# Kernel optimization log

Measured on AMD Instinct MI355X. Metric: run time of the kernel, lower is better.

The kernel has to match this reference:

```python
import jax, jax.numpy as jnp
import numpy as np

B, N, DIM = 4, 1024, 512
H, DH = 8, 64
INNER = H * DH
MLP = 2048
EPS = 1e-5


def layernorm(x, g, b):
    m = x.mean(-1, keepdims=True)
    v = ((x - m) ** 2).mean(-1, keepdims=True)
    return (x - m) / jnp.sqrt(v + EPS) * g + b


def setup_inputs() -> dict:
    key = jax.random.key(0)
    ks = jax.random.split(key, 12)
    s = 0.02
    return {
        "q": jax.random.normal(ks[0], (B, N, DIM), jnp.float32),
        "k": jax.random.normal(ks[1], (B, N, DIM), jnp.float32),
        "v": jax.random.normal(ks[2], (B, N, DIM), jnp.float32),
        "Win": jax.random.normal(ks[3], (INNER, DIM), jnp.float32) * s,
        "Wout": jax.random.normal(ks[4], (DIM, INNER), jnp.float32) * s,
        "bout": jnp.zeros((DIM,), jnp.float32),
        "g1": jnp.ones((DIM,), jnp.float32),
        "b1n": jnp.zeros((DIM,), jnp.float32),
        "g2": jnp.ones((DIM,), jnp.float32),
        "b2n": jnp.zeros((DIM,), jnp.float32),
        "Wup": jax.random.normal(ks[5], (MLP, DIM), jnp.float32) * s,
        "bup": jnp.zeros((MLP,), jnp.float32),
        "Wdn": jax.random.normal(ks[6], (DIM, MLP), jnp.float32) * s,
        "bdn": jnp.zeros((DIM,), jnp.float32),
        "wp_W1": jax.random.normal(ks[7], (DH, 2 * DH), jnp.float32) * s,
        "wp_b1": jnp.zeros((DH,), jnp.float32),
        "wp_g": jnp.ones((DH,), jnp.float32),
        "wp_b": jnp.zeros((DH,), jnp.float32),
        "wp_W2": jax.random.normal(ks[8], (3, DH), jnp.float32) * s,
        "wp_b2": jnp.zeros((3,), jnp.float32),
        "num_heads": H,
        "dim_head": DH,
        "mlp_dim": MLP,
    }


def reference(q, k, v, Win, Wout, bout, g1, b1n, g2, b2n, Wup, bup, Wdn, bdn,
              wp_W1, wp_b1, wp_g, wp_b, wp_W2, wp_b2, num_heads, dim_head, mlp_dim):
    b, n, _ = q.shape

    def split_heads(x):  # [b,n,dim] -> [h,b,n,d]
        f = x @ Win.T
        return f.reshape(b, n, num_heads, dim_head).transpose(2, 0, 1, 3)

    fq = split_heads(layernorm(q, g1, b1n))
    fk = split_heads(layernorm(k, g1, b1n))
    fv = split_heads(layernorm(v, g1, b1n))

    # cosine similarity component
    dots = jnp.einsum('hbnd,hbmd->hbnm', fq, fk)
    nq = jnp.linalg.norm(fq, axis=-1)  # [h,b,n]
    nk = jnp.linalg.norm(fk, axis=-1)  # [h,b,m]
    cosine_sim = dots / (nq[..., :, None] * nk[..., None, :])

    # mean-centered covariance component
    qc = fq - fq.mean(-1, keepdims=True)
    kc = fk - fk.mean(-1, keepdims=True)
    cov_component = jnp.einsum('hbnd,hbmd->hbnm', qc, kc) / dim_head

    # variance outer-product component (torch.var -> unbiased, ddof=1)
    qv = jnp.var(fq, axis=-1, ddof=1)  # [h,b,n]
    kv = jnp.var(fk, axis=-1, ddof=1)  # [h,b,m]
    var_component = qv[..., :, None] * kv[..., None, :] / dim_head

    # dynamic per-head mixing weights
    qg = fq.mean(axis=(1, 2))  # [h,d]
    kg = fk.mean(axis=(1, 2))
    feats = jnp.concatenate([qg, kg], axis=-1)  # [h,2d]
    h1 = jax.nn.relu(layernorm(feats @ wp_W1.T + wp_b1, wp_g, wp_b))
    w = jax.nn.softmax(h1 @ wp_W2.T + wp_b2, axis=-1)  # [h,3]
    cw = w[:, 0][:, None, None, None]
    covw = w[:, 1][:, None, None, None]
    vw = w[:, 2][:, None, None, None]

    scores = cw * cosine_sim + covw * cov_component + vw * var_component
    out = jnp.einsum('hbnm,hbmd->hbnd', scores, fv)
    out = out.transpose(1, 2, 0, 3).reshape(b, n, num_heads * dim_head)
    attn = out @ Wout.T + bout

    q2 = q + attn
    x = layernorm(q2, g2, b2n)
    y = jax.nn.gelu(x @ Wup.T + bup, approximate=False) @ Wdn.T + bdn
    return q2 + y
```

## Files before the change

### kernel.cpp

```cpp
#include <hip/hip_runtime.h>
#include <math.h>

#define EPS 1e-5f
#define ROWS 4096

typedef __attribute__((ext_vector_type(8))) short short8;
typedef __attribute__((ext_vector_type(4))) float floatx4;

__device__ inline short f2bf(float f) {
    unsigned u = __builtin_bit_cast(unsigned, f);
    unsigned r = (u + 0x7fffu + ((u >> 16) & 1u)) >> 16;
    return (short)r;
}
__device__ inline float bf2f(short s) {
    return __builtin_bit_cast(float, (unsigned)(unsigned short)s << 16);
}

__global__ __launch_bounds__(256) void prep(
    const float* __restrict__ q, const float* __restrict__ k,
    const float* __restrict__ v, const float* __restrict__ g,
    const float* __restrict__ bb, short* __restrict__ qkvout,
    const float* __restrict__ w0, const float* __restrict__ w1,
    const float* __restrict__ w2, const float* __restrict__ w3,
    short* __restrict__ o0, short* __restrict__ o1,
    short* __restrict__ o2, short* __restrict__ o3,
    const float* __restrict__ g2, const float* __restrict__ b2n,
    float* __restrict__ Bn, float* __restrict__ Wg,
    float* __restrict__ zero0) {
    int bx = blockIdx.x;
    int t = threadIdx.x;
    if (bx < 3072) {
        int tensor = bx >> 10;
        int xb = bx & 1023;
        const float* x = tensor == 0 ? q : (tensor == 1 ? k : v);
        int row = xb * 4 + (t >> 6);
        int col = (t & 63) * 8;
        const float* xr = x + (size_t)row * 512 + col;
        float4 v0 = *(const float4*)xr;
        float4 v1 = *(const float4*)(xr + 4);
        float s = v0.x + v0.y + v0.z + v0.w + v1.x + v1.y + v1.z + v1.w;
        float sq = v0.x * v0.x + v0.y * v0.y + v0.z * v0.z + v0.w * v0.w +
                   v1.x * v1.x + v1.y * v1.y + v1.z * v1.z + v1.w * v1.w;
#pragma unroll
        for (int off = 32; off; off >>= 1) {
            s += __shfl_xor(s, off);
            sq += __shfl_xor(sq, off);
        }
        float m = s * (1.f / 512.f);
        float rstd = rsqrtf(sq * (1.f / 512.f) - m * m + EPS);
        float4 g0 = *(const float4*)(g + col);
        float4 g1 = *(const float4*)(g + col + 4);
        float4 b0 = *(const float4*)(bb + col);
        float4 b1 = *(const float4*)(bb + col + 4);
        short8 o;
        o[0] = f2bf((v0.x - m) * rstd * g0.x + b0.x);
        o[1] = f2bf((v0.y - m) * rstd * g0.y + b0.y);
        o[2] = f2bf((v0.z - m) * rstd * g0.z + b0.z);
        o[3] = f2bf((v0.w - m) * rstd * g0.w + b0.w);
        o[4] = f2bf((v1.x - m) * rstd * g1.x + b1.x);
        o[5] = f2bf((v1.y - m) * rstd * g1.y + b1.y);
        o[6] = f2bf((v1.z - m) * rstd * g1.z + b1.z);
        o[7] = f2bf((v1.w - m) * rstd * g1.w + b1.w);
        *(short8*)(qkvout + (size_t)(tensor * 4096 + row) * 512 + col) = o;
        return;
    }
    if (bx < 4352) {
        int wb = bx - 3072;
        if (wb >= 256 && wb < 768) {
            int base = wb - 256;
            int idx = base * 2048 + t * 8;
            int n = idx >> 9, c = idx & 511;
            float4 v0 = *(const float4*)(w2 + idx);
            float4 v1 = *(const float4*)(w2 + idx + 4);
            float4 ga = *(const float4*)(g2 + c);
            float4 gb = *(const float4*)(g2 + c + 4);
            float4 ba = *(const float4*)(b2n + c);
            float4 bbv = *(const float4*)(b2n + c + 4);
            short8 o;
            o[0] = f2bf(ga.x * v0.x); o[1] = f2bf(ga.y * v0.y);
            o[2] = f2bf(ga.z * v0.z); o[3] = f2bf(ga.w * v0.w);
            o[4] = f2bf(gb.x * v1.x); o[5] = f2bf(gb.y * v1.y);
            o[6] = f2bf(gb.z * v1.z); o[7] = f2bf(gb.w * v1.w);
            *(short8*)(o2 + idx) = o;
            float bn = ba.x * v0.x + ba.y * v0.y + ba.z * v0.z + ba.w * v0.w +
                       bbv.x * v1.x + bbv.y * v1.y + bbv.z * v1.z + bbv.w * v1.w;
            float wg = ga.x * v0.x + ga.y * v0.y + ga.z * v0.z + ga.w * v0.w +
                       gb.x * v1.x + gb.y * v1.y + gb.z * v1.z + gb.w * v1.w;
#pragma unroll
            for (int off = 32; off; off >>= 1) {
                bn += __shfl_xor(bn, off);
                wg += __shfl_xor(wg, off);
            }
            if ((t & 63) == 0) {
                Bn[n] = bn;
                Wg[n] = wg;
            }
            return;
        }
        const float* src;
        short* dst;
        int base;
        if (wb < 128) { src = w0; dst = o0; base = wb; }
        else if (wb < 256) { src = w1; dst = o1; base = wb - 128; }
        else { src = w3; dst = o3; base = wb - 768; }
        int idx = base * 2048 + t * 8;
        float4 v0 = *(const float4*)(src + idx);
        float4 v1 = *(const float4*)(src + idx + 4);
        short8 o;
        o[0] = f2bf(v0.x); o[1] = f2bf(v0.y); o[2] = f2bf(v0.z); o[3] = f2bf(v0.w);
        o[4] = f2bf(v1.x); o[5] = f2bf(v1.y); o[6] = f2bf(v1.z); o[7] = f2bf(v1.w);
        *(short8*)(dst + idx) = o;
        return;
    }
    int zi = (bx - 4352) * 1024 + t * 4;
    if (zi < 275456) *(float4*)(zero0 + zi) = (float4){0.f, 0.f, 0.f, 0.f};
}

template <int TM, int TN, int EPI, bool OUT_BF16>
__global__ __launch_bounds__(256) void mfma_gemm_nt(
    const short* __restrict__ A, const short* __restrict__ B,
    void* __restrict__ C, int M, int N, int K,
    const float* __restrict__ bias, const float* __restrict__ resid,
    short* __restrict__ C2, float* __restrict__ Sb,
    float* __restrict__ qgp, float* __restrict__ kgp) {
    constexpr int FI = TM / 32;
    constexpr int FJ = TN / 32;
    __shared__ short As[2][TM * 32];
    __shared__ short Bs[2][TN * 32];
    int t = threadIdx.x;
    int m0 = blockIdx.y * TM, n0 = blockIdx.x * TN;
    int w = t >> 6, lane = t & 63;
    int wm = (w & 1) * (TM / 2), wn = (w >> 1) * (TN / 2);
    floatx4 acc[FI][FJ];
#pragma unroll
    for (int i = 0; i < FI; ++i)
#pragma unroll
        for (int j = 0; j < FJ; ++j) acc[i][j] = (floatx4){0.f, 0.f, 0.f, 0.f};

    int arow = t >> 2, acol = (t & 3) * 8;
    const short* Ag = A + (size_t)(m0 + arow) * K + acol;
    const short* Bg = B + (size_t)(n0 + arow) * K + acol;
    int ldsbase = w * 1024;

    auto stage = [&](int k0, int buf) {
#pragma unroll
        for (int u = 0; u < TM / 64; ++u)
            __builtin_amdgcn_global_load_lds(
                (const __attribute__((address_space(1))) void*)(Ag + (size_t)u * 64 * K + k0),
                (__attribute__((address_space(3))) void*)((char*)As[buf] + u * 4096 + ldsbase),
                16, 0, 0);
#pragma unroll
        for (int u = 0; u < TN / 64; ++u)
            __builtin_amdgcn_global_load_lds(
                (const __attribute__((address_space(1))) void*)(Bg + (size_t)u * 64 * K + k0),
                (__attribute__((address_space(3))) void*)((char*)Bs[buf] + u * 4096 + ldsbase),
                16, 0, 0);
    };

    stage(0, 0);
    __syncthreads();
    int nsteps = K >> 5;
    for (int ks = 0; ks < nsteps; ++ks) {
        int buf = ks & 1;
        if (ks + 1 < nsteps) stage((ks + 1) << 5, buf ^ 1);
        int krow = (lane >> 4) * 8;
        short8 af[FI], bf[FJ];
#pragma unroll
        for (int i = 0; i < FI; ++i)
            af[i] = *(const short8*)&As[buf][(wm + i * 16 + (lane & 15)) * 32 + krow];
#pragma unroll
        for (int j = 0; j < FJ; ++j)
            bf[j] = *(const short8*)&Bs[buf][(wn + j * 16 + (lane & 15)) * 32 + krow];
#pragma unroll
        for (int i = 0; i < FI; ++i)
#pragma unroll
            for (int j = 0; j < FJ; ++j)
                acc[i][j] = __builtin_amdgcn_mfma_f32_16x16x32_bf16(
                    af[i], bf[j], acc[i][j], 0, 0, 0);
        __syncthreads();
    }

    int col = lane & 15, rbase = (lane >> 4) * 4;
    if constexpr (EPI == 5) {
#pragma unroll
        for (int i = 0; i < FI; ++i) {
#pragma unroll
            for (int r = 0; r < 4; ++r) {
                int grow = m0 + wm + i * 16 + rbase + r;
                float s = 0.f, sq = 0.f;
#pragma unroll
                for (int j = 0; j < FJ; ++j) {
                    int gcol = n0 + wn + j * 16 + col;
                    float vv = acc[i][j][r] + bias[gcol] +
                               resid[(size_t)grow * N + gcol];
                    ((float*)C)[(size_t)grow * N + gcol] = vv;
                    C2[(size_t)grow * N + gcol] = f2bf(vv);
                    s += vv;
                    sq += vv * vv;
                }
#pragma unroll
                for (int off = 1; off < 16; off <<= 1) {
                    s += __shfl_xor(s, off);
                    sq += __shfl_xor(sq, off);
                }
                if ((lane & 15) == 0) {
                    atomicAdd(&Sb[grow], s);
                    atomicAdd(&Sb[4096 + grow], sq);
                }
            }
        }
    } else if constexpr (EPI == 4) {
#pragma unroll
        for (int i = 0; i < FI; ++i) {
#pragma unroll
            for (int r = 0; r < 4; ++r) {
                int grow = m0 + wm + i * 16 + rbase + r;
                float m = Sb[grow] * (1.f / 512.f);
                float rstd = rsqrtf(Sb[4096 + grow] * (1.f / 512.f) - m * m + EPS);
                float mrstd = m * rstd;
#pragma unroll
                for (int j = 0; j < FJ; ++j) {
                    int gcol = n0 + wn + j * 16 + col;
                    float vv = rstd * acc[i][j][r] + qgp[gcol] + bias[gcol] -
                               mrstd * kgp[gcol];
                    vv = 0.5f * vv * (1.f + erff(vv * 0.70710678118654752f));
                    ((short*)C)[(size_t)grow * N + gcol] = f2bf(vv);
                }
            }
        }
    } else {
#pragma unroll
        for (int i = 0; i < FI; ++i) {
#pragma unroll
            for (int j = 0; j < FJ; ++j) {
                int gcol = n0 + wn + j * 16 + col;
#pragma unroll
                for (int r = 0; r < 4; ++r) {
                    int grow = m0 + wm + i * 16 + rbase + r;
                    float v = acc[i][j][r];
                    if (EPI == 2) v += bias[gcol] + resid[(size_t)grow * N + gcol];
                    if (OUT_BF16)
                        ((short*)C)[(size_t)grow * N + gcol] = f2bf(v);
                    else
                        ((float*)C)[(size_t)grow * N + gcol] = v;
                }
            }
        }
    }

    if constexpr (EPI == 1) {
        if (m0 < 8192) {
            int tensor = m0 >> 12;
            float* Sbase = Sb + (size_t)tensor * 98304;
            float* dst = tensor ? kgp : qgp;
            int head = (n0 + wn) >> 6;
            int rowbase = (m0 & 4095) + wm;
#pragma unroll
            for (int i = 0; i < FI; ++i) {
#pragma unroll
                for (int r = 0; r < 4; ++r) {
                    float s = 0.f, sq = 0.f;
#pragma unroll
                    for (int j = 0; j < FJ; ++j) {
                        float vv = acc[i][j][r];
                        s += vv;
                        sq += vv * vv;
                    }
#pragma unroll
                    for (int off = 1; off < 16; off <<= 1) {
                        s += __shfl_xor(s, off);
                        sq += __shfl_xor(sq, off);
                    }
                    if ((lane & 15) == 0) {
                        int row = rowbase + i * 16 + rbase + r;
                        int idx = head * ROWS + row;
                        float m = s * (1.f / 64.f);
                        Sbase[idx] = m;
                        Sbase[32768 + idx] = rsqrtf(sq);
                        Sbase[65536 + idx] = (sq - 64.f * m * m) * (1.f / 63.f);
                    }
                }
            }
            float cs[FJ];
#pragma unroll
            for (int j = 0; j < FJ; ++j) {
                float s = 0.f;
#pragma unroll
                for (int i = 0; i < FI; ++i)
#pragma unroll
                    for (int r = 0; r < 4; ++r) s += acc[i][j][r];
                s += __shfl_xor(s, 16);
                s += __shfl_xor(s, 32);
                cs[j] = s;
            }
            if (lane < 16) {
#pragma unroll
                for (int j = 0; j < FJ; ++j)
                    atomicAdd(&dst[head * 64 + j * 16 + lane], cs[j] * (1.f / 4096.f));
            }
        }
    }
}

__global__ __launch_bounds__(256) void tr_kv(
    const short* __restrict__ fkb, const short* __restrict__ fvb,
    const float* __restrict__ rnk, const float* __restrict__ kvv,
    const float* __restrict__ mkm, short* __restrict__ fkTall,
    short* __restrict__ fvT, float* __restrict__ Sv,
    const float* __restrict__ qg, const float* __restrict__ kg,
    const float* __restrict__ W1, const float* __restrict__ b1,
    const float* __restrict__ g, const float* __restrict__ bb,
    const float* __restrict__ W2, const float* __restrict__ b2,
    float* __restrict__ wmix) {
    int hb = blockIdx.x;
    int t = threadIdx.x;
    if (blockIdx.y == 8) {
        if (blockIdx.z != 0 || hb >= 8 || t >= 64) return;
        int h = hb, j = t;
        float acc = 0.f;
        const float* w1r = W1 + j * 128;
        for (int i = 0; i < 64; ++i) acc += qg[h * 64 + i] * w1r[i];
        for (int i = 0; i < 64; ++i) acc += kg[h * 64 + i] * w1r[64 + i];
        acc += b1[j];
        float s = acc, sq = acc * acc;
#pragma unroll
        for (int off = 32; off; off >>= 1) {
            s += __shfl_xor(s, off);
            sq += __shfl_xor(sq, off);
        }
        float m = s * (1.f / 64.f);
        float var = sq * (1.f / 64.f) - m * m;
        float xh = (acc - m) * rsqrtf(var + EPS) * g[j] + bb[j];
        float r = fmaxf(xh, 0.f);
        float l[3];
#pragma unroll
        for (int c = 0; c < 3; ++c) {
            float p = r * W2[c * 64 + j];
#pragma unroll
            for (int off = 32; off; off >>= 1) p += __shfl_xor(p, off);
            l[c] = p + b2[c];
        }
        if (j == 0) {
            float mx = fmaxf(l[0], fmaxf(l[1], l[2]));
            float e0 = expf(l[0] - mx), e1 = expf(l[1] - mx), e2 = expf(l[2] - mx);
            float inv = 1.f / (e0 + e1 + e2);
            wmix[h * 3 + 0] = e0 * inv;
            wmix[h * 3 + 1] = e1 * inv;
            wmix[h * 3 + 2] = e2 * inv;
        }
        return;
    }
    int chunk = blockIdx.y;
    int tensor = blockIdx.z;
    int h = hb >> 2, b = hb & 3;
    __shared__ float tile[32][68];
    __shared__ float sc[32], sc2[32];
    const short* src = tensor ? fvb : fkb;
    float skv_acc = 0.f, smk_acc = 0.f;
    int e = t & 63, qd = t >> 6;
    int d = t >> 2, mg = (t & 3) * 8;
    for (int s4 = 0; s4 < 4; ++s4) {
        int m0 = chunk * 128 + s4 * 32;
        __syncthreads();
        {
            int idx = t * 8;
            int mm = idx >> 6, dd = idx & 63;
            short8 sv = *(const short8*)&src[(size_t)(b * 1024 + m0 + mm) * 512 + h * 64 + dd];
#pragma unroll
            for (int i = 0; i < 8; ++i) tile[mm][dd + i] = bf2f(sv[i]);
        }
        if (t < 32) {
            int sidx = h * ROWS + b * 1024 + m0 + t;
            if (tensor == 0) {
                sc[t] = rnk[sidx];
            } else {
                sc[t] = kvv[sidx];
                sc2[t] = mkm[sidx];
            }
        }
        __syncthreads();
        if (tensor == 0) {
            short8 o1, o2;
#pragma unroll
            for (int i = 0; i < 8; ++i) {
                float vv = tile[mg + i][d];
                o1[i] = f2bf(vv);
                o2[i] = f2bf(vv * sc[mg + i]);
            }
            *(short8*)&fkTall[((size_t)hb * 128 + d) * 1024 + m0 + mg] = o1;
            *(short8*)&fkTall[((size_t)hb * 128 + 64 + d) * 1024 + m0 + mg] = o2;
        } else {
            short8 o1;
#pragma unroll
            for (int i = 0; i < 8; ++i) o1[i] = f2bf(tile[mg + i][d]);
            *(short8*)&fvT[((size_t)hb * 64 + d) * 1024 + m0 + mg] = o1;
#pragma unroll
            for (int i = 0; i < 8; ++i) {
                float vv = tile[qd * 8 + i][e];
                skv_acc += sc[qd * 8 + i] * vv;
                smk_acc += sc2[qd * 8 + i] * vv;
            }
        }
    }
    if (tensor == 1) {
        atomicAdd(&Sv[hb * 128 + e], skv_acc);
        atomicAdd(&Sv[hb * 128 + 64 + e], smk_acc);
    }
}

__global__ __launch_bounds__(256) void kside_gemm(
    const short* __restrict__ fkTall, const short* __restrict__ fvT,
    float* __restrict__ Mnew) {
    int hb = blockIdx.x, half = blockIdx.y, kz = blockIdx.z;
    const short* A = fkTall + ((size_t)hb * 128 + half * 64) * 1024 + kz * 256;
    const short* B = fvT + (size_t)hb * 64 * 1024 + kz * 256;
    __shared__ short As[2][64 * 32];
    __shared__ short Bs[2][64 * 32];
    int t = threadIdx.x;
    int w = t >> 6, lane = t & 63;
    int wm = (w & 1) * 32, wn = (w >> 1) * 32;
    floatx4 acc[2][2];
#pragma unroll
    for (int i = 0; i < 2; ++i)
#pragma unroll
        for (int j = 0; j < 2; ++j) acc[i][j] = (floatx4){0.f, 0.f, 0.f, 0.f};
    int arow = t >> 2, acol = (t & 3) * 8;
    const short* Ag = A + (size_t)arow * 1024 + acol;
    const short* Bg = B + (size_t)arow * 1024 + acol;
    int ldsbase = w * 1024;

    auto stage = [&](int k0, int buf) {
        __builtin_amdgcn_global_load_lds(
            (const __attribute__((address_space(1))) void*)(Ag + k0),
            (__attribute__((address_space(3))) void*)((char*)As[buf] + ldsbase), 16, 0, 0);
        __builtin_amdgcn_global_load_lds(
            (const __attribute__((address_space(1))) void*)(Bg + k0),
            (__attribute__((address_space(3))) void*)((char*)Bs[buf] + ldsbase), 16, 0, 0);
    };

    stage(0, 0);
    __syncthreads();
    for (int ks = 0; ks < 8; ++ks) {
        int buf = ks & 1;
        if (ks + 1 < 8) stage((ks + 1) << 5, buf ^ 1);
        int krow = (lane >> 4) * 8;
        short8 af[2], bf[2];
#pragma unroll
        for (int i = 0; i < 2; ++i)
            af[i] = *(const short8*)&As[buf][(wm + i * 16 + (lane & 15)) * 32 + krow];
#pragma unroll
        for (int j = 0; j < 2; ++j)
            bf[j] = *(const short8*)&Bs[buf][(wn + j * 16 + (lane & 15)) * 32 + krow];
#pragma unroll
        for (int i = 0; i < 2; ++i)
#pragma unroll
            for (int j = 0; j < 2; ++j)
                acc[i][j] = __builtin_amdgcn_mfma_f32_16x16x32_bf16(
                    af[i], bf[j], acc[i][j], 0, 0, 0);
        __syncthreads();
    }
    int col = lane & 15, rbase = (lane >> 4) * 4;
    float* Cb = Mnew + (size_t)hb * 8192 + half * 4096;
#pragma unroll
    for (int i = 0; i < 2; ++i)
#pragma unroll
        for (int j = 0; j < 2; ++j)
#pragma unroll
            for (int r = 0; r < 4; ++r)
                atomicAdd(&Cb[(wm + i * 16 + rbase + r) * 64 + wn + j * 16 + col],
                          acc[i][j][r]);
}

__global__ __launch_bounds__(256) void qside(
    const short* __restrict__ fqb, const float* __restrict__ Mnew,
    const float* __restrict__ Sv, const float* __restrict__ rnq,
    const float* __restrict__ mq, const float* __restrict__ qv,
    const float* __restrict__ wmix, short* __restrict__ attn_out) {
    int ntile = blockIdx.x, hb = blockIdx.y;
    int h = hb >> 2, b = hb & 3;
    __shared__ float M1s[4096], M2s[4096], fqt[4096];
    __shared__ float Skvs[64], Smks[64], rnqs[64], mqs[64], qvs[64];
    int t = threadIdx.x;
    const float* base = Mnew + (size_t)hb * 8192;
#pragma unroll
    for (int u = 0; u < 4; ++u) {
        int idx = t * 4 + u * 1024;
        *(float4*)&M2s[idx] = *(const float4*)&base[idx];
        *(float4*)&M1s[idx] = *(const float4*)&base[4096 + idx];
    }
    int n0 = ntile * 64;
#pragma unroll
    for (int u = 0; u < 2; ++u) {
        int idx = t * 8 + u * 2048;
        int r = idx >> 6, d = idx & 63;
        short8 sv = *(const short8*)&fqb[(size_t)(b * 1024 + n0 + r) * 512 + h * 64 + d];
#pragma unroll
        for (int i = 0; i < 8; ++i) fqt[idx + i] = bf2f(sv[i]);
    }
    if (t < 64) {
        Skvs[t] = Sv[hb * 128 + t];
        Smks[t] = Sv[hb * 128 + 64 + t];
        int sidx = h * ROWS + b * 1024 + n0 + t;
        rnqs[t] = rnq[sidx];
        mqs[t] = mq[sidx];
        qvs[t] = qv[sidx];
    }
    __syncthreads();
    float cw = wmix[h * 3 + 0], covw = wmix[h * 3 + 1], vw = wmix[h * 3 + 2];
    int e = t & 63, rq = t >> 6;
    float a1[16] = {}, a2[16] = {};
    for (int d4 = 0; d4 < 64; d4 += 4) {
        float md1[4], md2[4];
#pragma unroll
        for (int dd = 0; dd < 4; ++dd) {
            md1[dd] = M1s[(d4 + dd) * 64 + e];
            md2[dd] = M2s[(d4 + dd) * 64 + e];
        }
#pragma unroll
        for (int i = 0; i < 16; ++i) {
            float4 f = *(const float4*)&fqt[(rq * 16 + i) * 64 + d4];
            a1[i] += f.x * md1[0] + f.y * md1[1] + f.z * md1[2] + f.w * md1[3];
            a2[i] += f.x * md2[0] + f.y * md2[1] + f.z * md2[2] + f.w * md2[3];
        }
    }
    float c2 = covw * (1.f / 64.f), c3 = vw * (1.f / 64.f);
#pragma unroll
    for (int i = 0; i < 16; ++i) {
        int rr = rq * 16 + i;
        float v = cw * rnqs[rr] * a1[i] + c2 * a2[i] + c3 * qvs[rr] * Skvs[e] -
                  covw * mqs[rr] * Smks[e];
        attn_out[(size_t)(b * 1024 + n0 + rr) * 512 + h * 64 + e] = f2bf(v);
    }
}

extern "C" void kernel_launch(void* const* d_in, const int* in_sizes, int n_in,
                              void* d_out, int out_size, void* d_ws, size_t ws_size,
                              hipStream_t stream) {
    const float* q = (const float*)d_in[0];
    const float* k = (const float*)d_in[1];
    const float* v = (const float*)d_in[2];
    const float* Win = (const float*)d_in[3];
    const float* Wout = (const float*)d_in[4];
    const float* bout = (const float*)d_in[5];
    const float* g1 = (const float*)d_in[6];
    const float* b1n = (const float*)d_in[7];
    const float* g2 = (const float*)d_in[8];
    const float* b2n = (const float*)d_in[9];
    const float* Wup = (const float*)d_in[10];
    const float* bup = (const float*)d_in[11];
    const float* Wdn = (const float*)d_in[12];
    const float* bdn = (const float*)d_in[13];
    const float* wpW1 = (const float*)d_in[14];
    const float* wpb1 = (const float*)d_in[15];
    const float* wpg = (const float*)d_in[16];
    const float* wpb = (const float*)d_in[17];
    const float* wpW2 = (const float*)d_in[18];
    const float* wpb2 = (const float*)d_in[19];
    float* out = (float*)d_out;

    float* wsf = (float*)d_ws;
    short* fqkv = (short*)wsf;
    short* fkb = fqkv + (size_t)4096 * 512;
    short* fvb = fqkv + (size_t)8192 * 512;
    short* qkvln = (short*)(wsf + 3145728);
    short* hmid = (short*)wsf;
    short* fkTall = (short*)(wsf + 4194304);
    short* attnbf = (short*)(wsf + 4194304);
    short* fvT = (short*)(wsf + 6291456);
    short* q2bf = (short*)(wsf + 7340032);
    short* Winbf = (short*)(wsf + 8388608);
    short* Woutbf = (short*)(wsf + 8388608 + 131072);
    short* Wupbf = (short*)(wsf + 8388608 + 262144);
    short* Wdnbf = (short*)(wsf + 8388608 + 262144 + 524288);
    float* S = wsf + 9699328;
    float* qg = S + 196608;
    float* kg = qg + 512;
    float* Mnew = kg + 512;
    float* Sv = Mnew + 262144;
    float* rowstats = Sv + 4096;
    float* wmix = rowstats + 8192;
    float* Bn = wmix + 32;
    float* Wg = Bn + 2048;
    float* mqS = S, *rnqS = S + 32768, *qvS = S + 65536;
    float* mkS = S + 98304, *rnkS = S + 131072, *kvS = S + 163840;

    prep<<<4621, 256, 0, stream>>>(q, k, v, g1, b1n, qkvln,
                                   Win, Wout, Wup, Wdn,
                                   Winbf, Woutbf, Wupbf, Wdnbf,
                                   g2, b2n, Bn, Wg, qg);

    mfma_gemm_nt<64, 128, 1, true><<<dim3(4, 192), 256, 0, stream>>>(
        qkvln, Winbf, fqkv, 12288, 512, 512, nullptr, nullptr, nullptr,
        S, qg, kg);

    tr_kv<<<dim3(32, 9, 2), 256, 0, stream>>>(fkb, fvb, rnkS, kvS, mkS,
                                              fkTall, fvT, Sv,
                                              qg, kg, wpW1, wpb1, wpg, wpb,
                                              wpW2, wpb2, wmix);

    kside_gemm<<<dim3(32, 2, 4), 256, 0, stream>>>(fkTall, fvT, Mnew);

    qside<<<dim3(16, 32), 256, 0, stream>>>(fqkv, Mnew, Sv, rnqS, mqS, qvS,
                                            wmix, attnbf);

    mfma_gemm_nt<64, 64, 5, false><<<dim3(8, 64), 256, 0, stream>>>(
        attnbf, Woutbf, out, 4096, 512, 512, bout, q, q2bf,
        rowstats, nullptr, nullptr);

    mfma_gemm_nt<64, 128, 4, true><<<dim3(16, 64), 256, 0, stream>>>(
        q2bf, Wupbf, hmid, 4096, 2048, 512, bup, nullptr, nullptr,
        rowstats, Bn, Wg);

    mfma_gemm_nt<64, 128, 2, false><<<dim3(4, 64), 256, 0, stream>>>(
        hmid, Wdnbf, out, 4096, 512, 2048, bdn, out, nullptr,
        nullptr, nullptr, nullptr);
}
```

Baseline: 233.7 us.

## Split-K the down-projection GEMM with atomic accumulation and enlarge up-projection tile

The down-projection GEMM (K=2048) is split into two K-halves across blockIdx.z. Each half atomically adds its partial sums into the residual output buffer, and only the first half adds the bias. This doubles the block count from 256 to 512 to raise occupancy on a GEMM that was under-filled. A separate leading-dimension parameter is added so strided K-slices can be read. The up-projection GEMM switches to a 128x128 tile, halving its grid. The atomics add memory traffic and make the summation order nondeterministic.

```diff
diff --git a/kernel.cpp b/kernel.cpp
--- a/kernel.cpp
+++ b/kernel.cpp
@@ -119,7 +119,7 @@
 template <int TM, int TN, int EPI, bool OUT_BF16>
 __global__ __launch_bounds__(256) void mfma_gemm_nt(
     const short* __restrict__ A, const short* __restrict__ B,
-    void* __restrict__ C, int M, int N, int K,
+    void* __restrict__ C, int M, int N, int K, int ldk,
     const float* __restrict__ bias, const float* __restrict__ resid,
     short* __restrict__ C2, float* __restrict__ Sb,
     float* __restrict__ qgp, float* __restrict__ kgp) {
@@ -131,6 +131,10 @@
     int m0 = blockIdx.y * TM, n0 = blockIdx.x * TN;
     int w = t >> 6, lane = t & 63;
     int wm = (w & 1) * (TM / 2), wn = (w >> 1) * (TN / 2);
+    if constexpr (EPI == 6) {
+        A += (size_t)blockIdx.z * K;
+        B += (size_t)blockIdx.z * K;
+    }
     floatx4 acc[FI][FJ];
 #pragma unroll
     for (int i = 0; i < FI; ++i)
@@ -138,21 +142,21 @@
         for (int j = 0; j < FJ; ++j) acc[i][j] = (floatx4){0.f, 0.f, 0.f, 0.f};
 
     int arow = t >> 2, acol = (t & 3) * 8;
-    const short* Ag = A + (size_t)(m0 + arow) * K + acol;
-    const short* Bg = B + (size_t)(n0 + arow) * K + acol;
+    const short* Ag = A + (size_t)(m0 + arow) * ldk + acol;
+    const short* Bg = B + (size_t)(n0 + arow) * ldk + acol;
     int ldsbase = w * 1024;
 
     auto stage = [&](int k0, int buf) {
 #pragma unroll
         for (int u = 0; u < TM / 64; ++u)
             __builtin_amdgcn_global_load_lds(
-                (const __attribute__((address_space(1))) void*)(Ag + (size_t)u * 64 * K + k0),
+                (const __attribute__((address_space(1))) void*)(Ag + (size_t)u * 64 * ldk + k0),
                 (__attribute__((address_space(3))) void*)((char*)As[buf] + u * 4096 + ldsbase),
                 16, 0, 0);
 #pragma unroll
         for (int u = 0; u < TN / 64; ++u)
             __builtin_amdgcn_global_load_lds(
-                (const __attribute__((address_space(1))) void*)(Bg + (size_t)u * 64 * K + k0),
+                (const __attribute__((address_space(1))) void*)(Bg + (size_t)u * 64 * ldk + k0),
                 (__attribute__((address_space(3))) void*)((char*)Bs[buf] + u * 4096 + ldsbase),
                 16, 0, 0);
     };
@@ -225,6 +229,22 @@
                                mrstd * kgp[gcol];
                     vv = 0.5f * vv * (1.f + erff(vv * 0.70710678118654752f));
                     ((short*)C)[(size_t)grow * N + gcol] = f2bf(vv);
+                }
+            }
+        }
+    } else if constexpr (EPI == 6) {
+        bool addb = (blockIdx.z == 0);
+#pragma unroll
+        for (int i = 0; i < FI; ++i) {
+#pragma unroll
+            for (int j = 0; j < FJ; ++j) {
+                int gcol = n0 + wn + j * 16 + col;
+                float bz = addb ? bias[gcol] : 0.f;
+#pragma unroll
+                for (int r = 0; r < 4; ++r) {
+                    int grow = m0 + wm + i * 16 + rbase + r;
+                    atomicAdd(&((float*)C)[(size_t)grow * N + gcol],
+                              acc[i][j][r] + bz);
                 }
             }
         }
@@ -590,7 +610,7 @@
                                    g2, b2n, Bn, Wg, qg);
 
     mfma_gemm_nt<64, 128, 1, true><<<dim3(4, 192), 256, 0, stream>>>(
-        qkvln, Winbf, fqkv, 12288, 512, 512, nullptr, nullptr, nullptr,
+        qkvln, Winbf, fqkv, 12288, 512, 512, 512, nullptr, nullptr, nullptr,
         S, qg, kg);
 
     tr_kv<<<dim3(32, 9, 2), 256, 0, stream>>>(fkb, fvb, rnkS, kvS, mkS,
@@ -604,14 +624,14 @@
                                             wmix, attnbf);
 
     mfma_gemm_nt<64, 64, 5, false><<<dim3(8, 64), 256, 0, stream>>>(
-        attnbf, Woutbf, out, 4096, 512, 512, bout, q, q2bf,
+        attnbf, Woutbf, out, 4096, 512, 512, 512, bout, q, q2bf,
         rowstats, nullptr, nullptr);
 
-    mfma_gemm_nt<64, 128, 4, true><<<dim3(16, 64), 256, 0, stream>>>(
-        q2bf, Wupbf, hmid, 4096, 2048, 512, bup, nullptr, nullptr,
+    mfma_gemm_nt<128, 128, 4, true><<<dim3(16, 32), 256, 0, stream>>>(
+        q2bf, Wupbf, hmid, 4096, 2048, 512, 512, bup, nullptr, nullptr,
         rowstats, Bn, Wg);
 
-    mfma_gemm_nt<64, 128, 2, false><<<dim3(4, 64), 256, 0, stream>>>(
-        hmid, Wdnbf, out, 4096, 512, 2048, bdn, out, nullptr,
+    mfma_gemm_nt<64, 128, 6, false><<<dim3(4, 64, 2), 256, 0, stream>>>(
+        hmid, Wdnbf, out, 4096, 512, 1024, 2048, bdn, nullptr, nullptr,
         nullptr, nullptr, nullptr);
 }
```

Result: no change. 235.8 us (+0.9%).

## Fuse K/V transpose and k-side GEMM into one kernel via LDS

Applied to the files above, without the earlier changes.

Merges the transpose kernel, which wrote transposed and scaled bf16 copies of fk/fv to global memory, with the k-side MFMA GEMM. The new kernel transposes each 32-row chunk in LDS and feeds MFMA directly, computing both the plain and rnk-scaled products in the same pass. This removes a global round-trip and one launch. The cost is a much smaller grid (132 blocks rather than 576+256) with synchronous, non-pipelined loads, so parallelism may drop. The GEMM kernel also gains an ldk stride parameter that is currently unused beyond K.

```diff
diff --git a/kernel.cpp b/kernel.cpp
--- a/kernel.cpp
+++ b/kernel.cpp
@@ -119,7 +119,7 @@
 template <int TM, int TN, int EPI, bool OUT_BF16>
 __global__ __launch_bounds__(256) void mfma_gemm_nt(
     const short* __restrict__ A, const short* __restrict__ B,
-    void* __restrict__ C, int M, int N, int K,
+    void* __restrict__ C, int M, int N, int K, int ldk,
     const float* __restrict__ bias, const float* __restrict__ resid,
     short* __restrict__ C2, float* __restrict__ Sb,
     float* __restrict__ qgp, float* __restrict__ kgp) {
@@ -138,21 +138,21 @@
         for (int j = 0; j < FJ; ++j) acc[i][j] = (floatx4){0.f, 0.f, 0.f, 0.f};
 
     int arow = t >> 2, acol = (t & 3) * 8;
-    const short* Ag = A + (size_t)(m0 + arow) * K + acol;
-    const short* Bg = B + (size_t)(n0 + arow) * K + acol;
+    const short* Ag = A + (size_t)(m0 + arow) * ldk + acol;
+    const short* Bg = B + (size_t)(n0 + arow) * ldk + acol;
     int ldsbase = w * 1024;
 
     auto stage = [&](int k0, int buf) {
 #pragma unroll
         for (int u = 0; u < TM / 64; ++u)
             __builtin_amdgcn_global_load_lds(
-                (const __attribute__((address_space(1))) void*)(Ag + (size_t)u * 64 * K + k0),
+                (const __attribute__((address_space(1))) void*)(Ag + (size_t)u * 64 * ldk + k0),
                 (__attribute__((address_space(3))) void*)((char*)As[buf] + u * 4096 + ldsbase),
                 16, 0, 0);
 #pragma unroll
         for (int u = 0; u < TN / 64; ++u)
             __builtin_amdgcn_global_load_lds(
-                (const __attribute__((address_space(1))) void*)(Bg + (size_t)u * 64 * K + k0),
+                (const __attribute__((address_space(1))) void*)(Bg + (size_t)u * 64 * ldk + k0),
                 (__attribute__((address_space(3))) void*)((char*)Bs[buf] + u * 4096 + ldsbase),
                 16, 0, 0);
     };
@@ -302,21 +302,22 @@
     }
 }
 
-__global__ __launch_bounds__(256) void tr_kv(
+__global__ __launch_bounds__(256) void kside_fused(
     const short* __restrict__ fkb, const short* __restrict__ fvb,
     const float* __restrict__ rnk, const float* __restrict__ kvv,
-    const float* __restrict__ mkm, short* __restrict__ fkTall,
-    short* __restrict__ fvT, float* __restrict__ Sv,
+    const float* __restrict__ mkm, float* __restrict__ Mnew,
+    float* __restrict__ Sv,
     const float* __restrict__ qg, const float* __restrict__ kg,
     const float* __restrict__ W1, const float* __restrict__ b1,
     const float* __restrict__ g, const float* __restrict__ bb,
     const float* __restrict__ W2, const float* __restrict__ b2,
     float* __restrict__ wmix) {
-    int hb = blockIdx.x;
     int t = threadIdx.x;
-    if (blockIdx.y == 8) {
-        if (blockIdx.z != 0 || hb >= 8 || t >= 64) return;
-        int h = hb, j = t;
+    if (blockIdx.x == 32) {
+        int wv = t >> 6;
+        if (wv >= 2) return;
+        int h = blockIdx.y * 2 + wv;
+        int j = t & 63;
         float acc = 0.f;
         const float* w1r = W1 + j * 128;
         for (int i = 0; i < 64; ++i) acc += qg[h * 64 + i] * w1r[i];
@@ -350,125 +351,93 @@
         }
         return;
     }
-    int chunk = blockIdx.y;
-    int tensor = blockIdx.z;
+    int hb = blockIdx.x, kz = blockIdx.y;
     int h = hb >> 2, b = hb & 3;
-    __shared__ float tile[32][68];
-    __shared__ float sc[32], sc2[32];
-    const short* src = tensor ? fvb : fkb;
-    float skv_acc = 0.f, smk_acc = 0.f;
-    int e = t & 63, qd = t >> 6;
-    int d = t >> 2, mg = (t & 3) * 8;
-    for (int s4 = 0; s4 < 4; ++s4) {
-        int m0 = chunk * 128 + s4 * 32;
-        __syncthreads();
-        {
-            int idx = t * 8;
-            int mm = idx >> 6, dd = idx & 63;
-            short8 sv = *(const short8*)&src[(size_t)(b * 1024 + m0 + mm) * 512 + h * 64 + dd];
-#pragma unroll
-            for (int i = 0; i < 8; ++i) tile[mm][dd + i] = bf2f(sv[i]);
-        }
-        if (t < 32) {
-            int sidx = h * ROWS + b * 1024 + m0 + t;
-            if (tensor == 0) {
-                sc[t] = rnk[sidx];
-            } else {
-                sc[t] = kvv[sidx];
-                sc2[t] = mkm[sidx];
-            }
-        }
-        __syncthreads();
-        if (tensor == 0) {
-            short8 o1, o2;
-#pragma unroll
-            for (int i = 0; i < 8; ++i) {
-                float vv = tile[mg + i][d];
-                o1[i] = f2bf(vv);
-                o2[i] = f2bf(vv * sc[mg + i]);
-            }
-            *(short8*)&fkTall[((size_t)hb * 128 + d) * 1024 + m0 + mg] = o1;
-            *(short8*)&fkTall[((size_t)hb * 128 + 64 + d) * 1024 + m0 + mg] = o2;
-        } else {
-            short8 o1;
-#pragma unroll
-            for (int i = 0; i < 8; ++i) o1[i] = f2bf(tile[mg + i][d]);
-            *(short8*)&fvT[((size_t)hb * 64 + d) * 1024 + m0 + mg] = o1;
-#pragma unroll
-            for (int i = 0; i < 8; ++i) {
-                float vv = tile[qd * 8 + i][e];
-                skv_acc += sc[qd * 8 + i] * vv;
-                smk_acc += sc2[qd * 8 + i] * vv;
-            }
-        }
-    }
-    if (tensor == 1) {
-        atomicAdd(&Sv[hb * 128 + e], skv_acc);
-        atomicAdd(&Sv[hb * 128 + 64 + e], smk_acc);
-    }
-}
-
-__global__ __launch_bounds__(256) void kside_gemm(
-    const short* __restrict__ fkTall, const short* __restrict__ fvT,
-    float* __restrict__ Mnew) {
-    int hb = blockIdx.x, half = blockIdx.y, kz = blockIdx.z;
-    const short* A = fkTall + ((size_t)hb * 128 + half * 64) * 1024 + kz * 256;
-    const short* B = fvT + (size_t)hb * 64 * 1024 + kz * 256;
-    __shared__ short As[2][64 * 32];
-    __shared__ short Bs[2][64 * 32];
-    int t = threadIdx.x;
+    __shared__ __attribute__((aligned(16))) short rawK[32 * 72];
+    __shared__ __attribute__((aligned(16))) short rawV[32 * 72];
+    __shared__ __attribute__((aligned(16))) short Ktp[64 * 40];
+    __shared__ __attribute__((aligned(16))) short Ktr[64 * 40];
+    __shared__ __attribute__((aligned(16))) short Vt[64 * 40];
+    __shared__ float rs[256], kvs[256], mks[256];
+    {
+        int sidx = h * ROWS + b * 1024 + kz * 256 + t;
+        rs[t] = rnk[sidx];
+        kvs[t] = kvv[sidx];
+        mks[t] = mkm[sidx];
+    }
     int w = t >> 6, lane = t & 63;
     int wm = (w & 1) * 32, wn = (w >> 1) * 32;
-    floatx4 acc[2][2];
+    floatx4 accP[2][2], accR[2][2];
 #pragma unroll
     for (int i = 0; i < 2; ++i)
 #pragma unroll
-        for (int j = 0; j < 2; ++j) acc[i][j] = (floatx4){0.f, 0.f, 0.f, 0.f};
-    int arow = t >> 2, acol = (t & 3) * 8;
-    const short* Ag = A + (size_t)arow * 1024 + acol;
-    const short* Bg = B + (size_t)arow * 1024 + acol;
-    int ldsbase = w * 1024;
-
-    auto stage = [&](int k0, int buf) {
-        __builtin_amdgcn_global_load_lds(
-            (const __attribute__((address_space(1))) void*)(Ag + k0),
-            (__attribute__((address_space(3))) void*)((char*)As[buf] + ldsbase), 16, 0, 0);
-        __builtin_amdgcn_global_load_lds(
-            (const __attribute__((address_space(1))) void*)(Bg + k0),
-            (__attribute__((address_space(3))) void*)((char*)Bs[buf] + ldsbase), 16, 0, 0);
-    };
-
-    stage(0, 0);
-    __syncthreads();
-    for (int ks = 0; ks < 8; ++ks) {
-        int buf = ks & 1;
-        if (ks + 1 < 8) stage((ks + 1) << 5, buf ^ 1);
-        int krow = (lane >> 4) * 8;
-        short8 af[2], bf[2];
+        for (int j = 0; j < 2; ++j) {
+            accP[i][j] = (floatx4){0.f, 0.f, 0.f, 0.f};
+            accR[i][j] = (floatx4){0.f, 0.f, 0.f, 0.f};
+        }
+    float skv_acc = 0.f, smk_acc = 0.f;
+    int mrow = t >> 3, dcol = (t & 7) * 8;
+    int dT = t >> 2, mg = (t & 3) * 8;
+    int krow = (lane >> 4) * 8;
+
+    for (int s = 0; s < 8; ++s) {
+        size_t gbase =
+            (size_t)(b * 1024 + kz * 256 + s * 32 + mrow) * 512 + h * 64 + dcol;
+        short8 k8 = *(const short8*)&fkb[gbase];
+        short8 v8 = *(const short8*)&fvb[gbase];
+        *(short8*)&rawK[mrow * 72 + dcol] = k8;
+        *(short8*)&rawV[mrow * 72 + dcol] = v8;
+        __syncthreads();
+        short8 okp, okr, ov;
+        int mb = s * 32 + mg;
+#pragma unroll
+        for (int i = 0; i < 8; ++i) {
+            short kv_ = rawK[(mg + i) * 72 + dT];
+            float kf = bf2f(kv_);
+            okp[i] = kv_;
+            okr[i] = f2bf(kf * rs[mb + i]);
+            short vv_ = rawV[(mg + i) * 72 + dT];
+            ov[i] = vv_;
+            float vf = bf2f(vv_);
+            skv_acc += kvs[mb + i] * vf;
+            smk_acc += mks[mb + i] * vf;
+        }
+        *(short8*)&Ktp[dT * 40 + mg] = okp;
+        *(short8*)&Ktr[dT * 40 + mg] = okr;
+        *(short8*)&Vt[dT * 40 + mg] = ov;
+        __syncthreads();
+        short8 afp[2], afr[2], bfv[2];
+#pragma unroll
+        for (int i = 0; i < 2; ++i) {
+            afp[i] = *(const short8*)&Ktp[(wm + i * 16 + (lane & 15)) * 40 + krow];
+            afr[i] = *(const short8*)&Ktr[(wm + i * 16 + (lane & 15)) * 40 + krow];
+            bfv[i] = *(const short8*)&Vt[(wn + i * 16 + (lane & 15)) * 40 + krow];
+        }
 #pragma unroll
         for (int i = 0; i < 2; ++i)
-            af[i] = *(const short8*)&As[buf][(wm + i * 16 + (lane & 15)) * 32 + krow];
+#pragma unroll
+            for (int j = 0; j < 2; ++j) {
+                accP[i][j] = __builtin_amdgcn_mfma_f32_16x16x32_bf16(
+                    afp[i], bfv[j], accP[i][j], 0, 0, 0);
+                accR[i][j] = __builtin_amdgcn_mfma_f32_16x16x32_bf16(
+                    afr[i], bfv[j], accR[i][j], 0, 0, 0);
+            }
+        __syncthreads();
+    }
+    int col = lane & 15, rbase = (lane >> 4) * 4;
+    float* Cb = Mnew + (size_t)hb * 8192;
+#pragma unroll
+    for (int i = 0; i < 2; ++i)
 #pragma unroll
         for (int j = 0; j < 2; ++j)
-            bf[j] = *(const short8*)&Bs[buf][(wn + j * 16 + (lane & 15)) * 32 + krow];
-#pragma unroll
-        for (int i = 0; i < 2; ++i)
-#pragma unroll
-            for (int j = 0; j < 2; ++j)
-                acc[i][j] = __builtin_amdgcn_mfma_f32_16x16x32_bf16(
-                    af[i], bf[j], acc[i][j], 0, 0, 0);
-        __syncthreads();
-    }
-    int col = lane & 15, rbase = (lane >> 4) * 4;
-    float* Cb = Mnew + (size_t)hb * 8192 + half * 4096;
-#pragma unroll
-    for (int i = 0; i < 2; ++i)
-#pragma unroll
-        for (int j = 0; j < 2; ++j)
-#pragma unroll
-            for (int r = 0; r < 4; ++r)
-                atomicAdd(&Cb[(wm + i * 16 + rbase + r) * 64 + wn + j * 16 + col],
-                          acc[i][j][r]);
+#pragma unroll
+            for (int r = 0; r < 4; ++r) {
+                int ci = (wm + i * 16 + rbase + r) * 64 + wn + j * 16 + col;
+                atomicAdd(&Cb[ci], accP[i][j][r]);
+                atomicAdd(&Cb[4096 + ci], accR[i][j][r]);
+            }
+    atomicAdd(&Sv[hb * 128 + dT], skv_acc);
+    atomicAdd(&Sv[hb * 128 + 64 + dT], smk_acc);
 }
 
 __global__ __launch_bounds__(256) void qside(
@@ -564,9 +533,7 @@
     short* fvb = fqkv + (size_t)8192 * 512;
     short* qkvln = (short*)(wsf + 3145728);
     short* hmid = (short*)wsf;
-    short* fkTall = (short*)(wsf + 4194304);
     short* attnbf = (short*)(wsf + 4194304);
-    short* fvT = (short*)(wsf + 6291456);
     short* q2bf = (short*)(wsf + 7340032);
     short* Winbf = (short*)(wsf + 8388608);
     short* Woutbf = (short*)(wsf + 8388608 + 131072);
@@ -590,28 +557,25 @@
                                    g2, b2n, Bn, Wg, qg);
 
     mfma_gemm_nt<64, 128, 1, true><<<dim3(4, 192), 256, 0, stream>>>(
-        qkvln, Winbf, fqkv, 12288, 512, 512, nullptr, nullptr, nullptr,
+        qkvln, Winbf, fqkv, 12288, 512, 512, 512, nullptr, nullptr, nullptr,
         S, qg, kg);
 
-    tr_kv<<<dim3(32, 9, 2), 256, 0, stream>>>(fkb, fvb, rnkS, kvS, mkS,
-                                              fkTall, fvT, Sv,
-                                              qg, kg, wpW1, wpb1, wpg, wpb,
-                                              wpW2, wpb2, wmix);
-
-    kside_gemm<<<dim3(32, 2, 4), 256, 0, stream>>>(fkTall, fvT, Mnew);
+    kside_fused<<<dim3(33, 4), 256, 0, stream>>>(
+        fkb, fvb, rnkS, kvS, mkS, Mnew, Sv,
+        qg, kg, wpW1, wpb1, wpg, wpb, wpW2, wpb2, wmix);
 
     qside<<<dim3(16, 32), 256, 0, stream>>>(fqkv, Mnew, Sv, rnqS, mqS, qvS,
                                             wmix, attnbf);
 
     mfma_gemm_nt<64, 64, 5, false><<<dim3(8, 64), 256, 0, stream>>>(
-        attnbf, Woutbf, out, 4096, 512, 512, bout, q, q2bf,
+        attnbf, Woutbf, out, 4096, 512, 512, 512, bout, q, q2bf,
         rowstats, nullptr, nullptr);
 
     mfma_gemm_nt<64, 128, 4, true><<<dim3(16, 64), 256, 0, stream>>>(
-        q2bf, Wupbf, hmid, 4096, 2048, 512, bup, nullptr, nullptr,
+        q2bf, Wupbf, hmid, 4096, 2048, 512, 512, bup, nullptr, nullptr,
         rowstats, Bn, Wg);
 
     mfma_gemm_nt<64, 128, 2, false><<<dim3(4, 64), 256, 0, stream>>>(
-        hmid, Wdnbf, out, 4096, 512, 2048, bdn, out, nullptr,
+        hmid, Wdnbf, out, 4096, 512, 2048, 2048, bdn, out, nullptr,
         nullptr, nullptr, nullptr);
 }
```

Result: no change. 233.3 us (median of 3 runs) (-0.2%).
